# Performance work log

Hardware: AMD Instinct MI355X
Metric: run time of the kernel (lower is better)

Reference implementation:

```python
import jax, jax.numpy as jnp
import numpy as np

B, S, D = 2, 2048, 2048
H, HD = 16, 128          # num_heads, head_dim (H*HD == D)
I = 4096                 # intermediate_size; ffn in-dim is 2*I
EPS = 1e-5


def rmsnorm(x, w):
    return x * jax.lax.rsqrt(jnp.mean(x * x, axis=-1, keepdims=True) + EPS) * w


def setup_inputs() -> dict:
    key = jax.random.key(0)
    ks = jax.random.split(key, 12)
    sd = 0.02
    return {
        "hidden_states": jax.random.normal(ks[0], (B, S, D), jnp.float32),
        "attention_mask": jnp.zeros((B, S), jnp.float32),  # additive mask
        "rn1_w": jnp.ones((D,), jnp.float32),
        "wq": jax.random.normal(ks[1], (D, D), jnp.float32) * sd,
        "wk": jax.random.normal(ks[2], (D, D), jnp.float32) * sd,
        "wv": jax.random.normal(ks[3], (D, D), jnp.float32) * sd,
        "wo": jax.random.normal(ks[4], (D, D), jnp.float32) * sd,
        "rn2_w": jnp.ones((D,), jnp.float32),
        "w1": jax.random.normal(ks[5], (D, 2 * I), jnp.float32) * sd,      # Linear(d, 2*I, bias=False)
        "fc1_w": jax.random.normal(ks[6], (2 * I, I), jnp.float32) * sd,   # SwiGLU fc1
        "fc1_b": jnp.zeros((I,), jnp.float32),
        "fc2_w": jax.random.normal(ks[7], (2 * I, I), jnp.float32) * sd,   # SwiGLU fc2
        "fc2_b": jnp.zeros((I,), jnp.float32),
        "w3": jax.random.normal(ks[8], (I, D), jnp.float32) * sd,          # Linear(I, d, bias=False)
    }


def reference(hidden_states, attention_mask, rn1_w, wq, wk, wv, wo, rn2_w,
              w1, fc1_w, fc1_b, fc2_w, fc2_b, w3):
    # --- attention ---
    attn_in = rmsnorm(hidden_states, rn1_w)
    q = (attn_in @ wq).reshape(B, S, H, HD)
    k = (attn_in @ wk).reshape(B, S, H, HD)
    v = (attn_in @ wv).reshape(B, S, H, HD)
    # rope_cache is None -> no rotary embedding applied
    scores = jnp.einsum("bqhd,bkhd->bhqk", q, k) / np.sqrt(HD).astype(np.float32)
    scores = scores + attention_mask[:, None, None, :]  # [B,1,1,S] broadcast
    probs = jax.nn.softmax(scores, axis=-1)             # dropout p=0 (eval)
    attn = jnp.einsum("bhqk,bkhd->bqhd", probs, v).reshape(B, S, D)
    residual1 = hidden_states + attn @ wo
    # --- SwiGLU FFN ---
    ffn_in = rmsnorm(residual1, rn2_w)
    x = ffn_in @ w1                                      # [B,S,2I]
    gated = jax.nn.silu(x @ fc1_w + fc1_b) * (x @ fc2_w + fc2_b)  # [B,S,I]
    return residual1 + gated @ w3
```

## Files before the change

kernel.cpp:

```cpp
#include <hip/hip_runtime.h>
#include <hip/hip_bf16.h>
#include <stdint.h>

using short8 = __attribute__((ext_vector_type(8))) short;
using uint4v = __attribute__((ext_vector_type(4))) unsigned int;
using f32x4  = __attribute__((ext_vector_type(4))) float;

#define DEV __device__ __forceinline__

DEV float b2f(unsigned short u) {
  union { unsigned int i; float f; } v; v.i = ((unsigned int)u) << 16; return v.f;
}
DEV unsigned short f2b(float f) {
  union { float f; unsigned int i; } v; v.f = f;
  unsigned int x = v.i;
  return (unsigned short)((x + 0x7FFFu + ((x >> 16) & 1u)) >> 16);
}
DEV void g2lds16(const void* g, void* l) {
  __builtin_amdgcn_global_load_lds((const __attribute__((address_space(1))) void*)g,
                                   (__attribute__((address_space(3))) void*)l, 16, 0, 0);
}

DEV void xcd_rect_map(int wg, int nbx, int rby, int rbx, int& by, int& bx) {
  const int xcd_cols = nbx / rbx;
  const int xcd = wg & 7, local = wg >> 3;
  const int xr = xcd / xcd_cols, xc = xcd % xcd_cols;
  by = xr * rby + local / rbx;
  bx = xc * rbx + local % rbx;
}

enum { EPI_BF16 = 0, EPI_RESID_F32 = 1, EPI_BIAS_BF16 = 2, EPI_RESID_OUT = 3, EPI_SWIGLU = 4 };

template<int EPI>
__global__ __launch_bounds__(512, 2)
void gemm_bt256(const unsigned short* __restrict__ A, const unsigned short* __restrict__ Bt,
                void* __restrict__ Cout, const void* __restrict__ extra,
                const void* __restrict__ extra2, int M, int N, int K, int rby, int rbx) {
  __shared__ __align__(16) unsigned short As[2][256 * 64];
  __shared__ __align__(16) unsigned short Bs[2][256 * 64];
  int by, bx;
  xcd_rect_map(blockIdx.x, N >> 8, rby, rbx, by, bx);
  const int m0 = by << 8, n0 = bx << 8;
  const int t = threadIdx.x;
  const int l = t & 63, wid = t >> 6;
  const int lr = l & 15, lg = l >> 4;
  const int wr = (wid >> 2) << 7;
  const int wc = (wid & 3) << 6;

  f32x4 acc[8][4];
#pragma unroll
  for (int i = 0; i < 8; ++i)
#pragma unroll
    for (int j = 0; j < 4; ++j) acc[i][j] = (f32x4){0.f, 0.f, 0.f, 0.f};

  const int sr = t >> 3;
  const int scSwz = ((t & 7) << 3) ^ ((sr & 7) << 3);
  const unsigned short* Ag = A  + (size_t)(m0 + sr) * K + scSwz;
  const unsigned short* Bg = Bt + (size_t)(n0 + sr) * K + scSwz;
  const int nT = K >> 6;

  const unsigned short* AgNext = Ag + 64;
  const unsigned short* BgNext = Bg + 64;
  const size_t rowK64 = (size_t)64 * K;

  const int xorv = (lr & 7) << 3;
  const int cb0 = (lg * 8) ^ xorv;
  const int cb1 = (32 + lg * 8) ^ xorv;

  short8 afA[2][2], afB[2][2], bfr[4][2];

#define STAGE_A(buf)                                                  \
  {                                                                   \
    unsigned short* dst = &As[buf][t * 8];                            \
    _Pragma("unroll")                                                 \
    for (int ld = 0; ld < 4; ++ld)                                    \
      g2lds16(AgNext + (size_t)ld * rowK64, dst + ld * 4096);         \
  }
#define STAGE_B(buf)                                                  \
  {                                                                   \
    unsigned short* dst = &Bs[buf][t * 8];                            \
    _Pragma("unroll")                                                 \
    for (int ld = 0; ld < 4; ++ld)                                    \
      g2lds16(BgNext + (size_t)ld * rowK64, dst + ld * 4096);         \
  }
#define READ_A(dst, base, p)                                          \
  {                                                                   \
    const int ro0 = (wr + ((p) * 2 + 0) * 16 + lr) << 6;              \
    const int ro1 = (wr + ((p) * 2 + 1) * 16 + lr) << 6;              \
    dst[0][0] = *(const short8*)((base) + ro0 + cb0);                 \
    dst[0][1] = *(const short8*)((base) + ro0 + cb1);                 \
    dst[1][0] = *(const short8*)((base) + ro1 + cb0);                 \
    dst[1][1] = *(const short8*)((base) + ro1 + cb1);                 \
  }
#define READ_B(base)                                                  \
  {                                                                   \
    _Pragma("unroll")                                                 \
    for (int ni = 0; ni < 4; ++ni) {                                  \
      const int ro = (wc + ni * 16 + lr) << 6;                        \
      bfr[ni][0] = *(const short8*)((base) + ro + cb0);               \
      bfr[ni][1] = *(const short8*)((base) + ro + cb1);               \
    }                                                                 \
  }
#define MFMA_PH(af, r0)                                               \
  {                                                                   \
    _Pragma("unroll")                                                 \
    for (int kk = 0; kk < 2; ++kk)                                    \
      _Pragma("unroll")                                               \
      for (int a = 0; a < 2; ++a)                                     \
        _Pragma("unroll")                                             \
        for (int ni = 0; ni < 4; ++ni)                                \
          acc[(r0) + a][ni] = __builtin_amdgcn_mfma_f32_16x16x32_bf16(\
              af[a][kk], bfr[ni][kk], acc[(r0) + a][ni], 0, 0, 0);    \
  }

  {
    unsigned short* dstA = &As[0][t * 8];
    unsigned short* dstB = &Bs[0][t * 8];
#pragma unroll
    for (int ld = 0; ld < 4; ++ld) {
      g2lds16(Ag + (size_t)ld * rowK64, dstA + ld * 4096);
      g2lds16(Bg + (size_t)ld * rowK64, dstB + ld * 4096);
    }
  }
  asm volatile("s_waitcnt vmcnt(0)\n\ts_barrier" ::: "memory");
  READ_A(afA, &As[0][0], 0);
  READ_B(&Bs[0][0]);

  for (int tt = 0; tt < nT; ++tt) {
    const unsigned short* base = &As[tt & 1][0];
    const int nb = (tt + 1) & 1;
    const bool more = (tt + 1) < nT;
    READ_A(afB, base, 1);
    if (more) STAGE_A(nb);
    asm volatile("s_waitcnt lgkmcnt(4)" ::: "memory");
    __builtin_amdgcn_sched_barrier(0);
    __builtin_amdgcn_s_setprio(1);
    MFMA_PH(afA, 0);
    __builtin_amdgcn_s_setprio(0);
    READ_A(afA, base, 2);
    if (more) STAGE_B(nb);
    asm volatile("s_waitcnt lgkmcnt(4)" ::: "memory");
    __builtin_amdgcn_sched_barrier(0);
    __builtin_amdgcn_s_setprio(1);
    MFMA_PH(afB, 2);
    __builtin_amdgcn_s_setprio(0);
    READ_A(afB, base, 3);
    asm volatile("s_waitcnt lgkmcnt(4)" ::: "memory");
    __builtin_amdgcn_sched_barrier(0);
    __builtin_amdgcn_s_setprio(1);
    MFMA_PH(afA, 4);
    __builtin_amdgcn_s_setprio(0);
    asm volatile("s_waitcnt lgkmcnt(0)" ::: "memory");
    __builtin_amdgcn_sched_barrier(0);
    __builtin_amdgcn_s_setprio(1);
    MFMA_PH(afB, 6);
    __builtin_amdgcn_s_setprio(0);
    asm volatile("s_waitcnt vmcnt(0)\n\ts_barrier" ::: "memory");
    if (more) {
      AgNext += 64;
      BgNext += 64;
      READ_A(afA, &As[nb][0], 0);
      READ_B(&Bs[nb][0]);
    }
  }
#undef STAGE_A
#undef STAGE_B
#undef READ_A
#undef READ_B
#undef MFMA_PH

#pragma unroll
  for (int mi = 0; mi < 8; ++mi) {
#pragma unroll
    for (int ni = 0; ni < 4; ++ni) {
      const int col = n0 + wc + ni * 16 + lr;
#pragma unroll
      for (int j = 0; j < 4; ++j) {
        const int row = m0 + wr + mi * 16 + lg * 4 + j;
        const size_t idx = (size_t)row * N + col;
        const float v = acc[mi][ni][j];
        if constexpr (EPI == EPI_BF16) {
          ((unsigned short*)Cout)[idx] = f2b(v);
        } else if constexpr (EPI == EPI_RESID_F32) {
          ((float*)Cout)[idx] = v + ((const float*)extra)[idx];
        } else if constexpr (EPI == EPI_BIAS_BF16) {
          ((unsigned short*)Cout)[idx] = f2b(v + ((const float*)extra)[col]);
        } else if constexpr (EPI == EPI_SWIGLU) {
          const float g1v = b2f(((const unsigned short*)extra2)[idx]);
          const float v2 = v + ((const float*)extra)[col];
          ((unsigned short*)Cout)[idx] = f2b(g1v / (1.f + __expf(-g1v)) * v2);
        } else {
          ((float*)Cout)[idx] = v + ((const float*)extra)[idx];
        }
      }
    }
  }
}

template<int EPI>
__global__ __launch_bounds__(256)
void gemm_bt(const unsigned short* __restrict__ A, const unsigned short* __restrict__ Bt,
             void* __restrict__ Cout, const void* __restrict__ extra,
             int M, int N, int K, int rby, int rbx) {
  __shared__ __align__(16) unsigned short As[128 * 64];
  __shared__ __align__(16) unsigned short Bs[128 * 64];
  int by, bx;
  xcd_rect_map(blockIdx.x, N >> 7, rby, rbx, by, bx);
  const int m0 = by << 7, n0 = bx << 7;
  const int t = threadIdx.x;
  const int l = t & 63, w = t >> 6;
  const int lr = l & 15, lg = l >> 4;
  const int wr = (w >> 1) << 6, wc = (w & 1) << 6;

  f32x4 acc[4][4];
#pragma unroll
  for (int i = 0; i < 4; ++i)
#pragma unroll
    for (int j = 0; j < 4; ++j) acc[i][j] = (f32x4){0.f, 0.f, 0.f, 0.f};

  const int sr = t >> 3;
  const int skSwz = ((t & 7) << 3) ^ ((sr & 7) << 3);
  const unsigned short* Ag = A  + (size_t)(m0 + sr) * K + skSwz;
  const unsigned short* Bg = Bt + (size_t)(n0 + sr) * K + skSwz;
  unsigned short* Al = As + t * 8;
  unsigned short* Bl = Bs + t * 8;

  for (int kt = 0; kt < K; kt += 64) {
#pragma unroll
    for (int c = 0; c < 4; ++c) {
      g2lds16(Ag + (size_t)(c * 32) * K + kt, Al + c * 2048);
      g2lds16(Bg + (size_t)(c * 32) * K + kt, Bl + c * 2048);
    }
    __syncthreads();
#pragma unroll
    for (int ks = 0; ks < 2; ++ks) {
      short8 af[4], bfr[4];
#pragma unroll
      for (int mi = 0; mi < 4; ++mi) {
        const int row = wr + mi * 16 + lr;
        af[mi] = *(const short8*)(As + (row << 6) + (((ks * 32 + lg * 8)) ^ ((row & 7) << 3)));
      }
#pragma unroll
      for (int ni = 0; ni < 4; ++ni) {
        const int row = wc + ni * 16 + lr;
        bfr[ni] = *(const short8*)(Bs + (row << 6) + (((ks * 32 + lg * 8)) ^ ((row & 7) << 3)));
      }
#pragma unroll
      for (int mi = 0; mi < 4; ++mi)
#pragma unroll
        for (int ni = 0; ni < 4; ++ni)
          acc[mi][ni] = __builtin_amdgcn_mfma_f32_16x16x32_bf16(af[mi], bfr[ni], acc[mi][ni], 0, 0, 0);
    }
    __syncthreads();
  }

#pragma unroll
  for (int mi = 0; mi < 4; ++mi) {
#pragma unroll
    for (int ni = 0; ni < 4; ++ni) {
      const int col = n0 + wc + ni * 16 + lr;
#pragma unroll
      for (int j = 0; j < 4; ++j) {
        const int row = m0 + wr + mi * 16 + lg * 4 + j;
        const size_t idx = (size_t)row * N + col;
        const float v = acc[mi][ni][j];
        if constexpr (EPI == EPI_BF16) {
          ((unsigned short*)Cout)[idx] = f2b(v);
        } else if constexpr (EPI == EPI_RESID_F32) {
          ((float*)Cout)[idx] = v + ((const float*)extra)[idx];
        } else if constexpr (EPI == EPI_BIAS_BF16) {
          ((unsigned short*)Cout)[idx] = f2b(v + ((const float*)extra)[col]);
        } else {
          ((float*)Cout)[idx] = v + ((const float*)extra)[idx];
        }
      }
    }
  }
}

__global__ __launch_bounds__(256)
void attn_fwd(const unsigned short* __restrict__ qkv, const unsigned short* __restrict__ vt,
              const float* __restrict__ mask, unsigned short* __restrict__ out) {
  __shared__ __align__(16) unsigned short Ks[64 * 128];
  __shared__ __align__(16) unsigned short Vs[128 * 64];
  __shared__ __align__(16) unsigned short Ps[4][16 * 64];
  const int b = blockIdx.z, hh = blockIdx.y;
  const int q0 = blockIdx.x << 6;
  const int t = threadIdx.x, l = t & 63, w = t >> 6;
  const int lr = l & 15, lg = l >> 4;
  const float scale = 0.08838834764831845f;

  short8 qf[4];
  {
    const unsigned short* qb = qkv + (size_t)(b * 2048 + q0 + w * 16 + lr) * 6144 + hh * 128;
#pragma unroll
    for (int ks = 0; ks < 4; ++ks) qf[ks] = *(const short8*)(qb + ks * 32 + lg * 8);
  }
  f32x4 acc_o[8];
#pragma unroll
  for (int i = 0; i < 8; ++i) acc_o[i] = (f32x4){0.f, 0.f, 0.f, 0.f};
  float m_r[4], l_r[4];
#pragma unroll
  for (int j = 0; j < 4; ++j) { m_r[j] = -1e30f; l_r[j] = 0.f; }

  const unsigned short* kb = qkv + (size_t)(b * 2048) * 6144 + 2048 + hh * 128;
  const unsigned short* vb = vt + (size_t)(b * 16 + hh) * 128 * 2048;
  const float* mb = mask + b * 2048;

  for (int kt = 0; kt < 2048; kt += 64) {
#pragma unroll
    for (int c = 0; c < 4; ++c) {
      const int e = (c * 256 + t) * 8;
      const int kr = e >> 7, kc = e & 127;
      g2lds16(kb + (size_t)(kt + kr) * 6144 + (kc ^ ((kr & 7) << 3)), Ks + e);
      const int vr = e >> 6, vc = e & 63;
      g2lds16(vb + (size_t)vr * 2048 + kt + (vc ^ ((vr & 7) << 3)), Vs + e);
    }
    __syncthreads();

    f32x4 sc[4];
#pragma unroll
    for (int nt = 0; nt < 4; ++nt) {
      f32x4 s = (f32x4){0.f, 0.f, 0.f, 0.f};
#pragma unroll
      for (int ks = 0; ks < 4; ++ks) {
        short8 kf = *(const short8*)(Ks + ((nt * 16 + lr) << 7) + ((ks * 32 + lg * 8) ^ ((lr & 7) << 3)));
        s = __builtin_amdgcn_mfma_f32_16x16x32_bf16(qf[ks], kf, s, 0, 0, 0);
      }
      sc[nt] = s;
    }
#pragma unroll
    for (int nt = 0; nt < 4; ++nt) {
      const float mv = mb[kt + nt * 16 + lr];
#pragma unroll
      for (int j = 0; j < 4; ++j) sc[nt][j] = sc[nt][j] * scale + mv;
    }
#pragma unroll
    for (int j = 0; j < 4; ++j) {
      float tm = fmaxf(fmaxf(sc[0][j], sc[1][j]), fmaxf(sc[2][j], sc[3][j]));
      tm = fmaxf(tm, __shfl_xor(tm, 1));
      tm = fmaxf(tm, __shfl_xor(tm, 2));
      tm = fmaxf(tm, __shfl_xor(tm, 4));
      tm = fmaxf(tm, __shfl_xor(tm, 8));
      const float mn = fmaxf(m_r[j], tm);
      const float corr = __expf(m_r[j] - mn);
      m_r[j] = mn;
      float ps = 0.f;
#pragma unroll
      for (int nt = 0; nt < 4; ++nt) {
        const float p = __expf(sc[nt][j] - mn);
        sc[nt][j] = p;
        ps += p;
      }
      ps += __shfl_xor(ps, 1);
      ps += __shfl_xor(ps, 2);
      ps += __shfl_xor(ps, 4);
      ps += __shfl_xor(ps, 8);
      l_r[j] = l_r[j] * corr + ps;
#pragma unroll
      for (int di = 0; di < 8; ++di) acc_o[di][j] *= corr;
    }
#pragma unroll
    for (int nt = 0; nt < 4; ++nt)
#pragma unroll
      for (int j = 0; j < 4; ++j) {
        const int q = lg * 4 + j;
        Ps[w][(q << 6) + ((nt * 16 + lr) ^ ((q & 7) << 3))] = f2b(sc[nt][j]);
      }
    asm volatile("s_waitcnt lgkmcnt(0)" ::: "memory");
#pragma unroll
    for (int ks2 = 0; ks2 < 2; ++ks2) {
      short8 pf = *(const short8*)(&Ps[w][(lr << 6) + ((ks2 * 32 + lg * 8) ^ ((lr & 7) << 3))]);
#pragma unroll
      for (int di = 0; di < 8; ++di) {
        short8 vf = *(const short8*)(Vs + ((di * 16 + lr) << 6) + ((ks2 * 32 + lg * 8) ^ ((lr & 7) << 3)));
        acc_o[di] = __builtin_amdgcn_mfma_f32_16x16x32_bf16(pf, vf, acc_o[di], 0, 0, 0);
      }
    }
    __syncthreads();
  }
#pragma unroll
  for (int di = 0; di < 8; ++di)
#pragma unroll
    for (int j = 0; j < 4; ++j) {
      const int q = q0 + w * 16 + lg * 4 + j;
      out[(size_t)(b * 2048 + q) * 2048 + hh * 128 + di * 16 + lr] = f2b(acc_o[di][j] / l_r[j]);
    }
}

__global__ __launch_bounds__(256)
void rmsnorm_k(const float* __restrict__ in, const float* __restrict__ wgt,
               unsigned short* __restrict__ out) {
  __shared__ float red[4];
  const int row = blockIdx.x, t = threadIdx.x;
  const float4* rp = (const float4*)(in + (size_t)row * 2048 + t * 8);
  float4 a = rp[0], b = rp[1];
  float x[8] = {a.x, a.y, a.z, a.w, b.x, b.y, b.z, b.w};
  float s = 0.f;
#pragma unroll
  for (int i = 0; i < 8; ++i) s += x[i] * x[i];
#pragma unroll
  for (int m = 1; m < 64; m <<= 1) s += __shfl_xor(s, m);
  const int l = t & 63, w = t >> 6;
  if (l == 0) red[w] = s;
  __syncthreads();
  const float tot = red[0] + red[1] + red[2] + red[3];
  const float rr = rsqrtf(tot * (1.f / 2048.f) + 1e-5f);
  const float4* wp = (const float4*)(wgt + t * 8);
  float4 wa = wp[0], wb = wp[1];
  float ww[8] = {wa.x, wa.y, wa.z, wa.w, wb.x, wb.y, wb.z, wb.w};
  short8 o;
#pragma unroll
  for (int i = 0; i < 8; ++i) o[i] = (short)f2b(x[i] * rr * ww[i]);
  *(short8*)(out + (size_t)row * 2048 + t * 8) = o;
}

__global__ __launch_bounds__(256)
void transpose2d(const float* __restrict__ in, unsigned short* __restrict__ out,
                 int R, int C) {
  __shared__ __align__(16) unsigned int tile2[64][36];
  const int r0 = blockIdx.y << 6, c0 = blockIdx.x << 6;
  const int t = threadIdx.x;
#pragma unroll
  for (int it = 0; it < 2; ++it) {
    const int p = it * 256 + t;
    const int r2 = p >> 4;
    const int c = (p & 15) << 2;
    const float* src = in + (size_t)(r0 + r2 * 2) * C + c0 + c;
    float4 va = *(const float4*)(src);
    float4 vb = *(const float4*)(src + C);
    tile2[c + 0][r2] = (unsigned int)f2b(va.x) | ((unsigned int)f2b(vb.x) << 16);
    tile2[c + 1][r2] = (unsigned int)f2b(va.y) | ((unsigned int)f2b(vb.y) << 16);
    tile2[c + 2][r2] = (unsigned int)f2b(va.z) | ((unsigned int)f2b(vb.z) << 16);
    tile2[c + 3][r2] = (unsigned int)f2b(va.w) | ((unsigned int)f2b(vb.w) << 16);
  }
  __syncthreads();
#pragma unroll
  for (int it = 0; it < 2; ++it) {
    const int u = it * 256 + t;
    const int rr = u >> 3;
    const int k8 = u & 7;
    uint4v v = *(const uint4v*)(&tile2[rr][k8 * 4]);
    short8 o;
#pragma unroll
    for (int j = 0; j < 4; ++j) {
      o[2 * j]     = (short)(v[j] & 0xFFFFu);
      o[2 * j + 1] = (short)(v[j] >> 16);
    }
    *(short8*)(out + (size_t)(c0 + rr) * R + r0 + k8 * 8) = o;
  }
}

__global__ __launch_bounds__(256)
void transpose_v(const unsigned short* __restrict__ qkv, unsigned short* __restrict__ vt) {
  __shared__ __align__(16) unsigned short tile[64][72];
  const int s0 = blockIdx.x << 6, d0 = blockIdx.y << 6;
  const int z = blockIdx.z;
  const unsigned short* in = qkv + (size_t)((z >> 4) * 2048) * 6144 + 4096 + (z & 15) * 128;
  unsigned short* outp = vt + (size_t)z * 128 * 2048;
  const int t = threadIdx.x;
#pragma unroll
  for (int it = 0; it < 2; ++it) {
    const int e = (it * 256 + t) * 8;
    const int r = e >> 6, cc = e & 63;
    short8 v = *(const short8*)(in + (size_t)(s0 + r) * 6144 + d0 + cc);
#pragma unroll
    for (int i = 0; i < 8; ++i) tile[cc + i][r] = (unsigned short)v[i];
  }
  __syncthreads();
#pragma unroll
  for (int it = 0; it < 2; ++it) {
    const int e = (it * 256 + t) * 8;
    const int rr = e >> 6, kk = e & 63;
    short8 v = *(const short8*)(&tile[rr][kk]);
    *(short8*)(outp + (size_t)(d0 + rr) * 2048 + s0 + kk) = v;
  }
}

extern "C" void kernel_launch(void* const* d_in, const int* in_sizes, int n_in,
                              void* d_out, int out_size, void* d_ws, size_t ws_size,
                              hipStream_t stream) {
  const float* h    = (const float*)d_in[0];
  const float* mask = (const float*)d_in[1];
  const float* rn1w = (const float*)d_in[2];
  const float* wq   = (const float*)d_in[3];
  const float* wk   = (const float*)d_in[4];
  const float* wv   = (const float*)d_in[5];
  const float* wo   = (const float*)d_in[6];
  const float* rn2w = (const float*)d_in[7];
  const float* w1   = (const float*)d_in[8];
  const float* fc1w = (const float*)d_in[9];
  const float* fc1b = (const float*)d_in[10];
  const float* fc2w = (const float*)d_in[11];
  const float* fc2b = (const float*)d_in[12];
  const float* w3   = (const float*)d_in[13];

  char* ws = (char*)d_ws;
  size_t off = 0;
  auto alloc = [&](size_t bytes) { char* p = ws + off; off += (bytes + 255) & ~(size_t)255; return p; };
  unsigned short* bufA = (unsigned short*)alloc(16777216);
  unsigned short* bufB = (unsigned short*)alloc(16777216);
  unsigned short* qkv  = (unsigned short*)alloc(50331648);
  float*          r1f  = (float*)alloc(33554432);
  unsigned short* xbuf = (unsigned short*)alloc(67108864);
  unsigned short* g1   = (unsigned short*)alloc(33554432);
  unsigned short* wt   = (unsigned short*)alloc(67108864);
  if (off > ws_size) return;

  rmsnorm_k<<<4096, 256, 0, stream>>>(h, rn1w, bufA);
  transpose2d<<<dim3(32, 32), 256, 0, stream>>>(wq, wt,                 2048, 2048);
  transpose2d<<<dim3(32, 32), 256, 0, stream>>>(wk, wt + 2048 * 2048,   2048, 2048);
  transpose2d<<<dim3(32, 32), 256, 0, stream>>>(wv, wt + 2 * 2048 * 2048, 2048, 2048);
  gemm_bt256<EPI_BF16><<<384, 512, 0, stream>>>(bufA, wt, qkv, nullptr, nullptr, 4096, 6144, 2048, 8, 6);
  transpose_v<<<dim3(32, 2, 32), 256, 0, stream>>>(qkv, bufB);
  attn_fwd<<<dim3(32, 16, 2), 256, 0, stream>>>(qkv, bufB, mask, bufA);
  transpose2d<<<dim3(32, 32), 256, 0, stream>>>(wo, wt, 2048, 2048);
  gemm_bt<EPI_RESID_F32><<<512, 256, 0, stream>>>(bufA, wt, r1f, h, 4096, 2048, 2048, 8, 8);

  rmsnorm_k<<<4096, 256, 0, stream>>>(r1f, rn2w, bufB);
  transpose2d<<<dim3(128, 32), 256, 0, stream>>>(w1, wt, 2048, 8192);
  gemm_bt256<EPI_BF16><<<512, 512, 0, stream>>>(bufB, wt, xbuf, nullptr, nullptr, 4096, 8192, 2048, 8, 8);
  transpose2d<<<dim3(64, 128), 256, 0, stream>>>(fc1w, wt, 8192, 4096);
  gemm_bt256<EPI_BIAS_BF16><<<256, 512, 0, stream>>>(xbuf, wt, g1, fc1b, nullptr, 4096, 4096, 8192, 4, 8);
  transpose2d<<<dim3(64, 128), 256, 0, stream>>>(fc2w, wt, 8192, 4096);
  unsigned short* gated = qkv;
  gemm_bt256<EPI_SWIGLU><<<256, 512, 0, stream>>>(xbuf, wt, gated, fc2b, g1, 4096, 4096, 8192, 4, 8);
  transpose2d<<<dim3(32, 64), 256, 0, stream>>>(w3, wt, 4096, 2048);
  gemm_bt<EPI_RESID_OUT><<<512, 256, 0, stream>>>(gated, wt, d_out, r1f, 4096, 2048, 4096, 8, 8);
}
```

Measured before the change: 1.162 ms.

## Switch GEMM inner loop to 32x32x16 bf16 MFMA with simplified two-phase schedule

Replaces the 16x16x32 MFMA tiling with 32x32x16 MFMA instructions, reorganizing LDS fragment reads, accumulator layout (f32x16) and epilogue row/column mapping. The larger MFMA shape cuts the number of fragment loads from LDS per FLOP and the instruction count. The main loop is simplified into two phases with full lgkmcnt(0) waits and no cross-iteration prefetch of fragments, which may expose LDS latency that the previous finer interleaving hid.

```diff
diff --git a/kernel.cpp b/kernel.cpp
--- a/kernel.cpp
+++ b/kernel.cpp
@@ -5,6 +5,7 @@
 using short8 = __attribute__((ext_vector_type(8))) short;
 using uint4v = __attribute__((ext_vector_type(4))) unsigned int;
 using f32x4  = __attribute__((ext_vector_type(4))) float;
+using f32x16 = __attribute__((ext_vector_type(16))) float;
 
 #define DEV __device__ __forceinline__
 
@@ -43,15 +44,18 @@
   const int m0 = by << 8, n0 = bx << 8;
   const int t = threadIdx.x;
   const int l = t & 63, wid = t >> 6;
-  const int lr = l & 15, lg = l >> 4;
+  const int l31 = l & 31;
+  const int hi8 = (l >> 5) << 3;
   const int wr = (wid >> 2) << 7;
   const int wc = (wid & 3) << 6;
 
-  f32x4 acc[8][4];
-#pragma unroll
-  for (int i = 0; i < 8; ++i)
-#pragma unroll
-    for (int j = 0; j < 4; ++j) acc[i][j] = (f32x4){0.f, 0.f, 0.f, 0.f};
+  f32x16 acc[4][2];
+#pragma unroll
+  for (int i = 0; i < 4; ++i)
+#pragma unroll
+    for (int j = 0; j < 2; ++j)
+#pragma unroll
+      for (int r = 0; r < 16; ++r) acc[i][j][r] = 0.f;
 
   const int sr = t >> 3;
   const int scSwz = ((t & 7) << 3) ^ ((sr & 7) << 3);
@@ -63,11 +67,7 @@
   const unsigned short* BgNext = Bg + 64;
   const size_t rowK64 = (size_t)64 * K;
 
-  const int xorv = (lr & 7) << 3;
-  const int cb0 = (lg * 8) ^ xorv;
-  const int cb1 = (32 + lg * 8) ^ xorv;
-
-  short8 afA[2][2], afB[2][2], bfr[4][2];
+  short8 af[2][4], bfr[2][4];
 
 #define STAGE_A(buf)                                                  \
   {                                                                   \
@@ -83,34 +83,40 @@
     for (int ld = 0; ld < 4; ++ld)                                    \
       g2lds16(BgNext + (size_t)ld * rowK64, dst + ld * 4096);         \
   }
-#define READ_A(dst, base, p)                                          \
+#define READ_A2(base, mi0)                                            \
   {                                                                   \
-    const int ro0 = (wr + ((p) * 2 + 0) * 16 + lr) << 6;              \
-    const int ro1 = (wr + ((p) * 2 + 1) * 16 + lr) << 6;              \
-    dst[0][0] = *(const short8*)((base) + ro0 + cb0);                 \
-    dst[0][1] = *(const short8*)((base) + ro0 + cb1);                 \
-    dst[1][0] = *(const short8*)((base) + ro1 + cb0);                 \
-    dst[1][1] = *(const short8*)((base) + ro1 + cb1);                 \
+    _Pragma("unroll")                                                 \
+    for (int a = 0; a < 2; ++a) {                                     \
+      const int row = wr + ((mi0) + a) * 32 + l31;                    \
+      const int ro = row << 6;                                        \
+      const int sw = (row & 7) << 3;                                  \
+      _Pragma("unroll")                                               \
+      for (int ks = 0; ks < 4; ++ks)                                  \
+        af[a][ks] = *(const short8*)((base) + ro + ((ks * 16 + hi8) ^ sw)); \
+    }                                                                 \
   }
 #define READ_B(base)                                                  \
   {                                                                   \
     _Pragma("unroll")                                                 \
-    for (int ni = 0; ni < 4; ++ni) {                                  \
-      const int ro = (wc + ni * 16 + lr) << 6;                        \
-      bfr[ni][0] = *(const short8*)((base) + ro + cb0);               \
-      bfr[ni][1] = *(const short8*)((base) + ro + cb1);               \
+    for (int ni = 0; ni < 2; ++ni) {                                  \
+      const int row = wc + ni * 32 + l31;                             \
+      const int ro = row << 6;                                        \
+      const int sw = (row & 7) << 3;                                  \
+      _Pragma("unroll")                                               \
+      for (int ks = 0; ks < 4; ++ks)                                  \
+        bfr[ni][ks] = *(const short8*)((base) + ro + ((ks * 16 + hi8) ^ sw)); \
     }                                                                 \
   }
-#define MFMA_PH(af, r0)                                               \
+#define MFMA_PH32(mi0)                                                \
   {                                                                   \
     _Pragma("unroll")                                                 \
-    for (int kk = 0; kk < 2; ++kk)                                    \
+    for (int ks = 0; ks < 4; ++ks)                                    \
       _Pragma("unroll")                                               \
       for (int a = 0; a < 2; ++a)                                     \
         _Pragma("unroll")                                             \
-        for (int ni = 0; ni < 4; ++ni)                                \
-          acc[(r0) + a][ni] = __builtin_amdgcn_mfma_f32_16x16x32_bf16(\
-              af[a][kk], bfr[ni][kk], acc[(r0) + a][ni], 0, 0, 0);    \
+        for (int ni = 0; ni < 2; ++ni)                                \
+          acc[(mi0) + a][ni] = __builtin_amdgcn_mfma_f32_32x32x16_bf16( \
+              af[a][ks], bfr[ni][ks], acc[(mi0) + a][ni], 0, 0, 0);   \
   }
 
   {
@@ -123,62 +129,47 @@
     }
   }
   asm volatile("s_waitcnt vmcnt(0)\n\ts_barrier" ::: "memory");
-  READ_A(afA, &As[0][0], 0);
-  READ_B(&Bs[0][0]);
 
   for (int tt = 0; tt < nT; ++tt) {
-    const unsigned short* base = &As[tt & 1][0];
+    const unsigned short* baseA = &As[tt & 1][0];
+    const unsigned short* baseB = &Bs[tt & 1][0];
     const int nb = (tt + 1) & 1;
     const bool more = (tt + 1) < nT;
-    READ_A(afB, base, 1);
     if (more) STAGE_A(nb);
-    asm volatile("s_waitcnt lgkmcnt(4)" ::: "memory");
-    __builtin_amdgcn_sched_barrier(0);
-    __builtin_amdgcn_s_setprio(1);
-    MFMA_PH(afA, 0);
-    __builtin_amdgcn_s_setprio(0);
-    READ_A(afA, base, 2);
-    if (more) STAGE_B(nb);
-    asm volatile("s_waitcnt lgkmcnt(4)" ::: "memory");
-    __builtin_amdgcn_sched_barrier(0);
-    __builtin_amdgcn_s_setprio(1);
-    MFMA_PH(afB, 2);
-    __builtin_amdgcn_s_setprio(0);
-    READ_A(afB, base, 3);
-    asm volatile("s_waitcnt lgkmcnt(4)" ::: "memory");
-    __builtin_amdgcn_sched_barrier(0);
-    __builtin_amdgcn_s_setprio(1);
-    MFMA_PH(afA, 4);
-    __builtin_amdgcn_s_setprio(0);
+    READ_B(baseB);
+    READ_A2(baseA, 0);
     asm volatile("s_waitcnt lgkmcnt(0)" ::: "memory");
     __builtin_amdgcn_sched_barrier(0);
     __builtin_amdgcn_s_setprio(1);
-    MFMA_PH(afB, 6);
+    MFMA_PH32(0);
+    __builtin_amdgcn_s_setprio(0);
+    if (more) STAGE_B(nb);
+    READ_A2(baseA, 2);
+    asm volatile("s_waitcnt lgkmcnt(0)" ::: "memory");
+    __builtin_amdgcn_sched_barrier(0);
+    __builtin_amdgcn_s_setprio(1);
+    MFMA_PH32(2);
     __builtin_amdgcn_s_setprio(0);
     asm volatile("s_waitcnt vmcnt(0)\n\ts_barrier" ::: "memory");
-    if (more) {
-      AgNext += 64;
-      BgNext += 64;
-      READ_A(afA, &As[nb][0], 0);
-      READ_B(&Bs[nb][0]);
-    }
+    if (more) { AgNext += 64; BgNext += 64; }
   }
 #undef STAGE_A
 #undef STAGE_B
-#undef READ_A
+#undef READ_A2
 #undef READ_B
-#undef MFMA_PH
-
-#pragma unroll
-  for (int mi = 0; mi < 8; ++mi) {
-#pragma unroll
-    for (int ni = 0; ni < 4; ++ni) {
-      const int col = n0 + wc + ni * 16 + lr;
-#pragma unroll
-      for (int j = 0; j < 4; ++j) {
-        const int row = m0 + wr + mi * 16 + lg * 4 + j;
+#undef MFMA_PH32
+
+  const int rbase = ((l >> 5) << 2);
+#pragma unroll
+  for (int mi = 0; mi < 4; ++mi) {
+#pragma unroll
+    for (int ni = 0; ni < 2; ++ni) {
+      const int col = n0 + wc + ni * 32 + l31;
+#pragma unroll
+      for (int reg = 0; reg < 16; ++reg) {
+        const int row = m0 + wr + mi * 32 + (reg & 3) + ((reg >> 2) << 3) + rbase;
         const size_t idx = (size_t)row * N + col;
-        const float v = acc[mi][ni][j];
+        const float v = acc[mi][ni][reg];
         if constexpr (EPI == EPI_BF16) {
           ((unsigned short*)Cout)[idx] = f2b(v);
         } else if constexpr (EPI == EPI_RESID_F32) {
```

Result: slower. 1.367 ms (+17.6%).
